# Performance work log

Measured on AMD Instinct MI355X. Metric: run time of the kernel, lower is better.

Reference implementation:

```python
import jax, jax.numpy as jnp
import numpy as np

N_PATHS = 8
T2_EFF = 0.5 * 100.0 + 0.5 * (100 // 50)  # p_dimer*T2_dimer + p_trimer*T2_trimer = 51.0
J_FREQ = 20.0


def setup_inputs() -> dict:
    key = jax.random.key(0)
    ks = jax.random.split(key, 5)
    B, D, H, P = 2048, 1024, 1024, N_PATHS
    return {
        "x": jax.random.normal(ks[0], (B, D), dtype=jnp.float32),
        "W_input": jax.random.normal(ks[1], (D, H), dtype=jnp.float32) * 0.1,
        "W_paths": jax.random.normal(ks[2], (P, H, H), dtype=jnp.float32) * 0.1,
        "J_coupling": jax.random.normal(ks[3], (P, P), dtype=jnp.float32) * 0.01,
        "coherent_state": jax.random.normal(ks[4], (B, P, H), dtype=jnp.float32),
        "t": jnp.ones((1,), dtype=jnp.float32),  # time_since_formation buffer
    }


def reference(x, W_input, W_paths, J_coupling, coherent_state, t):
    # base activation: [B, H]
    base = x @ W_input
    # all per-path matmuls batched into one einsum: [B, P, H]
    path_act = jnp.einsum("bh,phk->bpk", base, W_paths)
    # coherence decay gate (scalar, broadcasts)
    alpha = jnp.clip(jnp.exp(-t[0] / T2_EFF), 0.0, 1.0)
    superposition = alpha * coherent_state + (1.0 - alpha) * path_act
    # interference matrix from symmetrized J-coupling
    J_sym = 0.5 * (J_coupling + J_coupling.T)
    phase = 2.0 * jnp.pi * J_FREQ * t[0] / 1000.0
    interference = jax.nn.softmax(jnp.cos(phase * J_sym), axis=1)  # [P, P]
    # double-loop mixing == small matmul over path dim
    interfered = jnp.einsum("ij,bjh->bih", interference, superposition) / N_PATHS
    interfered = interfered * alpha  # coherence_factor == alpha
    # no measurement (default path): mean over paths
    return jnp.mean(interfered, axis=1)  # [B, H]
```

## Files before the change

### kernel.cpp

```cpp
#include <hip/hip_runtime.h>
#include <cstdint>


typedef __attribute__((ext_vector_type(8))) __bf16 bf16x8;
typedef __attribute__((ext_vector_type(4))) float f32x4;

__device__ __forceinline__ unsigned short f32_to_bf16_rne(float f) {
  unsigned int u = __float_as_uint(f);
  u += 0x7fffu + ((u >> 16) & 1u);
  return (unsigned short)(u >> 16);
}

__device__ __forceinline__ void load16_lds(const void* g, void* l) {
  __builtin_amdgcn_global_load_lds(
      (const __attribute__((address_space(1))) void*)g,
      (__attribute__((address_space(3))) void*)(unsigned int)(unsigned long long)l,
      16, 0, 0);
}

__device__ __forceinline__ void wave_scalars(const float* __restrict__ J,
                                             const float* __restrict__ t,
                                             float* w_out, float* alpha_out) {
  const int lane = threadIdx.x & 63;
  float tv = t[0];
  float alpha = fminf(fmaxf(expf(-tv / 51.0f), 0.0f), 1.0f);
  float phase = 2.0f * 3.14159265358979323846f * 20.0f * tv / 1000.0f;
  int i = lane >> 3, j = lane & 7;
  float jsym = 0.5f * (J[i * 8 + j] + J[j * 8 + i]);
  float e = expf(cosf(phase * jsym));
  float rs = e;
  rs += __shfl_xor(rs, 1);
  rs += __shfl_xor(rs, 2);
  rs += __shfl_xor(rs, 4);
  float p = e / rs;
  float cs = p;
  cs += __shfl_xor(cs, 8);
  cs += __shfl_xor(cs, 16);
  cs += __shfl_xor(cs, 32);
  *w_out = alpha * (1.0f / 64.0f) * cs;
  *alpha_out = alpha;
}

__global__ __launch_bounds__(256, 4) void k_prep(
    const float* __restrict__ x, const float* __restrict__ win,
    const float* __restrict__ wp, const float* __restrict__ J,
    const float* __restrict__ t, const float* __restrict__ coh,
    unsigned short* __restrict__ xb, unsigned short* __restrict__ winb,
    unsigned short* __restrict__ wefft, float* __restrict__ out) {
  const int blk = blockIdx.x;
  const int tid = threadIdx.x;
  const int lane = tid & 63;

  if (blk < 3072) {
    int idx = blk * 256 + tid;
    const float4* src;
    unsigned short* dst;
    int off;
    if (idx < 524288) { src = (const float4*)x;   dst = xb;   off = idx; }
    else              { src = (const float4*)win; dst = winb; off = idx - 524288; }
    float4 v = src[off];
    ushort4 o;
    o.x = f32_to_bf16_rne(v.x);
    o.y = f32_to_bf16_rne(v.y);
    o.z = f32_to_bf16_rne(v.z);
    o.w = f32_to_bf16_rne(v.w);
    ((ushort4*)dst)[off] = o;
  } else if (blk < 5120) {
    float wv, alpha;
    wave_scalars(J, t, &wv, &alpha);
    float wHI[8];
#pragma unroll
    for (int p = 0; p < 8; p++) wHI[p] = __shfl(wv, (lane & 56) | p) * alpha;
    int idx = (blk - 3072) * 256 + tid;
    int b = idx >> 8, hq = idx & 255;
    const f32x4* cb = (const f32x4*)(coh + (size_t)b * 8192) + hq;
    f32x4 acc = {0.f, 0.f, 0.f, 0.f};
#pragma unroll
    for (int p = 0; p < 8; p++) acc += wHI[p] * cb[p * 256];
    ((f32x4*)out)[idx] = acc;
  } else {
    __shared__ float lt[64][69];
    float wv, alpha;
    wave_scalars(J, t, &wv, &alpha);
    float wLO[8];
#pragma unroll
    for (int p = 0; p < 8; p++)
      wLO[p] = __shfl(wv, (lane & 56) | p) * (1.0f - alpha);
    const int q = blk - 5120;
    const int a0 = (q & 15) * 64;
    const int b0 = (q >> 4) * 64;
    const int rb = tid >> 4, c = tid & 15;
    f32x4 acc[4];
#pragma unroll
    for (int s = 0; s < 4; s++) acc[s] = {0.f, 0.f, 0.f, 0.f};
#pragma unroll
    for (int j = 0; j < 8; j++) {
      const float* base = wp + (size_t)j * 1024 * 1024 + b0 + c * 4;
      float wj = wLO[j];
#pragma unroll
      for (int s = 0; s < 4; s++) {
        f32x4 v = *(const f32x4*)(base + (size_t)(a0 + rb + 16 * s) * 1024);
        acc[s] += wj * v;
      }
    }
#pragma unroll
    for (int s = 0; s < 4; s++)
#pragma unroll
      for (int e = 0; e < 4; e++) lt[rb + 16 * s][c * 4 + e] = acc[s][e];
    __syncthreads();
    const int h2l = tid >> 2, h1g = (tid & 3) * 16;
    unsigned short* dst = wefft + (size_t)(b0 + h2l) * 1024 + a0 + h1g;
#pragma unroll
    for (int v4 = 0; v4 < 4; v4++) {
      ushort4 o;
      o.x = f32_to_bf16_rne(lt[h1g + v4 * 4 + 0][h2l]);
      o.y = f32_to_bf16_rne(lt[h1g + v4 * 4 + 1][h2l]);
      o.z = f32_to_bf16_rne(lt[h1g + v4 * 4 + 2][h2l]);
      o.w = f32_to_bf16_rne(lt[h1g + v4 * 4 + 3][h2l]);
      ((ushort4*)dst)[v4] = o;
    }
  }
}

template <int MAIN>
__global__ __launch_bounds__(256, 4) void k_gemm(
    const unsigned short* __restrict__ A, const unsigned short* __restrict__ B,
    float* __restrict__ outf, unsigned short* __restrict__ outb) {
  constexpr int K = 1024;
  constexpr int BK = 64;
  __shared__ alignas(16) unsigned short As[64 * BK];
  __shared__ alignas(16) unsigned short Bs[32 * BK];

  const int m0 = blockIdx.x * 64;
  const int n0 = blockIdx.y * 32;
  const int tid = threadIdx.x;
  const int wave = tid >> 6;
  const int lane = tid & 63;
  const int quad = lane >> 4;
  const int t16 = lane & 15;

  const int crow = lane >> 3;
  const int grp = lane & 7;
  const unsigned short* gA[2];
  unsigned short* lA[2];
#pragma unroll
  for (int c = 0; c < 2; c++) {
    int r = wave * 16 + c * 8 + crow;
    gA[c] = A + (size_t)(m0 + r) * K + (size_t)((grp ^ (r & 7)) * 8);
    lA[c] = As + (wave * 16 + c * 8) * BK + lane * 8;
  }
  const int rB = wave * 8 + crow;
  const unsigned short* gB = B + (size_t)(n0 + rB) * K + (size_t)((grp ^ (rB & 7)) * 8);
  unsigned short* lB = Bs + (wave * 8) * BK + lane * 8;

  const int ra = wave * 16 + t16;
  const unsigned short* pa[2];
  const unsigned short* pb[2][2];
#pragma unroll
  for (int kk = 0; kk < 2; kk++)
    pa[kk] = As + ra * BK + ((kk * 4 + quad) ^ (ra & 7)) * 8;
#pragma unroll
  for (int ni = 0; ni < 2; ni++) {
    int rb = ni * 16 + t16;
#pragma unroll
    for (int kk = 0; kk < 2; kk++)
      pb[ni][kk] = Bs + rb * BK + ((kk * 4 + quad) ^ (rb & 7)) * 8;
  }

  f32x4 acc[2] = {{0.f, 0.f, 0.f, 0.f}, {0.f, 0.f, 0.f, 0.f}};

  for (int kt = 0; kt < K; kt += BK) {
    __syncthreads();
    load16_lds(gA[0] + kt, lA[0]);
    load16_lds(gA[1] + kt, lA[1]);
    load16_lds(gB + kt, lB);
    __syncthreads();
#pragma unroll
    for (int kk = 0; kk < 2; kk++) {
      bf16x8 a = *(const bf16x8*)pa[kk];
      bf16x8 b0v = *(const bf16x8*)pb[0][kk];
      bf16x8 b1v = *(const bf16x8*)pb[1][kk];
      acc[0] = __builtin_amdgcn_mfma_f32_16x16x32_bf16(a, b0v, acc[0], 0, 0, 0);
      acc[1] = __builtin_amdgcn_mfma_f32_16x16x32_bf16(a, b1v, acc[1], 0, 0, 0);
    }
  }

#pragma unroll
  for (int r = 0; r < 4; r++) {
    const int m = m0 + wave * 16 + quad * 4 + r;
#pragma unroll
    for (int ni = 0; ni < 2; ni++) {
      const int n = n0 + ni * 16 + t16;
      const size_t idx = (size_t)m * 1024 + n;
      if constexpr (MAIN) {
        outf[idx] = outf[idx] + acc[ni][r];
      } else {
        outb[idx] = f32_to_bf16_rne(acc[ni][r]);
      }
    }
  }
}

extern "C" void kernel_launch(void* const* d_in, const int* in_sizes, int n_in,
                              void* d_out, int out_size, void* d_ws, size_t ws_size,
                              hipStream_t stream) {
  const float* x   = (const float*)d_in[0];
  const float* win = (const float*)d_in[1];
  const float* wp  = (const float*)d_in[2];
  const float* J   = (const float*)d_in[3];
  const float* coh = (const float*)d_in[4];
  const float* t   = (const float*)d_in[5];
  float* out = (float*)d_out;

  char* ws = (char*)d_ws;
  unsigned short* xb    = (unsigned short*)ws;
  unsigned short* winb  = (unsigned short*)(ws + 4u * 1024 * 1024);
  unsigned short* wefft = (unsigned short*)(ws + 6u * 1024 * 1024);
  unsigned short* wct   = (unsigned short*)(ws + 8u * 1024 * 1024);

  k_prep<<<5376, 256, 0, stream>>>(x, win, wp, J, t, coh, xb, winb, wefft, out);
  k_gemm<0><<<dim3(16, 32), 256, 0, stream>>>(wefft, winb, nullptr, wct);
  k_gemm<1><<<dim3(32, 32), 256, 0, stream>>>(xb, wct, out, nullptr);
}
```

Before: 162.3 us.

## Pre-swizzle bf16 operands into MFMA fragment layout and drop LDS staging in GEMMs

The prep kernel now writes x, W_input, the collapsed path weight and the intermediate product directly in a per-lane MFMA fragment order. This lets the GEMM kernels load bf16x8 operands straight from global memory with no LDS tiles or barriers. The GEMM tiles grow (64x64 and 128x64 per block, with several fragments per wave) and the prep grid is reduced by giving each block more work. The cost is extra LDS transposes in prep and reliance on cache for operand reuse across waves.

```diff
diff --git a/kernel.cpp b/kernel.cpp
--- a/kernel.cpp
+++ b/kernel.cpp
@@ -4,18 +4,12 @@
 
 typedef __attribute__((ext_vector_type(8))) __bf16 bf16x8;
 typedef __attribute__((ext_vector_type(4))) float f32x4;
-
-__device__ __forceinline__ unsigned short f32_to_bf16_rne(float f) {
+typedef unsigned short u16;
+
+__device__ __forceinline__ u16 f32_to_bf16_rne(float f) {
   unsigned int u = __float_as_uint(f);
   u += 0x7fffu + ((u >> 16) & 1u);
-  return (unsigned short)(u >> 16);
-}
-
-__device__ __forceinline__ void load16_lds(const void* g, void* l) {
-  __builtin_amdgcn_global_load_lds(
-      (const __attribute__((address_space(1))) void*)g,
-      (__attribute__((address_space(3))) void*)(unsigned int)(unsigned long long)l,
-      16, 0, 0);
+  return (u16)(u >> 16);
 }
 
 __device__ __forceinline__ void wave_scalars(const float* __restrict__ J,
@@ -41,162 +35,180 @@
   *alpha_out = alpha;
 }
 
-__global__ __launch_bounds__(256, 4) void k_prep(
+__global__ __launch_bounds__(256) void k_prep(
     const float* __restrict__ x, const float* __restrict__ win,
     const float* __restrict__ wp, const float* __restrict__ J,
     const float* __restrict__ t, const float* __restrict__ coh,
-    unsigned short* __restrict__ xb, unsigned short* __restrict__ winb,
-    unsigned short* __restrict__ wefft, float* __restrict__ out) {
+    u16* __restrict__ xfrag, u16* __restrict__ winfrag,
+    u16* __restrict__ wefrag, float* __restrict__ out) {
+  __shared__ __align__(16) char smem[33024];
   const int blk = blockIdx.x;
   const int tid = threadIdx.x;
   const int lane = tid & 63;
 
-  if (blk < 3072) {
-    int idx = blk * 256 + tid;
-    const float4* src;
-    unsigned short* dst;
-    int off;
-    if (idx < 524288) { src = (const float4*)x;   dst = xb;   off = idx; }
-    else              { src = (const float4*)win; dst = winb; off = idx - 524288; }
-    float4 v = src[off];
-    ushort4 o;
-    o.x = f32_to_bf16_rne(v.x);
-    o.y = f32_to_bf16_rne(v.y);
-    o.z = f32_to_bf16_rne(v.z);
-    o.w = f32_to_bf16_rne(v.w);
-    ((ushort4*)dst)[off] = o;
-  } else if (blk < 5120) {
+  if (blk < 256) {
+    float* lt = (float*)smem;
+    float wv, alpha;
+    wave_scalars(J, t, &wv, &alpha);
+    float wLO[8];
+#pragma unroll
+    for (int p = 0; p < 8; p++)
+      wLO[p] = __shfl(wv, (lane & 56) | p) * (1.0f - alpha);
+    const int a0 = (blk & 15) * 64;
+    const int b0 = (blk >> 4) * 64;
+    const int rb = tid >> 4, c = tid & 15;
+    f32x4 acc[4];
+#pragma unroll
+    for (int s = 0; s < 4; s++) acc[s] = (f32x4){0.f, 0.f, 0.f, 0.f};
+#pragma unroll
+    for (int j = 0; j < 8; j++) {
+      const float* base = wp + (size_t)j * 1048576 + b0 + c * 4;
+      float wj = wLO[j];
+#pragma unroll
+      for (int s = 0; s < 4; s++)
+        acc[s] += wj * *(const f32x4*)(base + (size_t)(a0 + rb + 16 * s) * 1024);
+    }
+#pragma unroll
+    for (int s = 0; s < 4; s++)
+#pragma unroll
+      for (int e = 0; e < 4; e++) lt[(rb + 16 * s) * 69 + c * 4 + e] = acc[s][e];
+    __syncthreads();
+#pragma unroll
+    for (int s2 = 0; s2 < 2; s2++) {
+      int idx = s2 * 256 + tid;
+      int lf = idx & 63, ktl = (idx >> 6) & 1, rtl = idx >> 7;
+      int h2l = rtl * 16 + (lf & 15);
+      int h1b = ktl * 32 + ((lf >> 4) << 3);
+      __align__(16) u16 o[8];
+#pragma unroll
+      for (int i = 0; i < 8; i++)
+        o[i] = f32_to_bf16_rne(lt[(h1b + i) * 69 + h2l]);
+      int rt = (b0 >> 4) + rtl, kt = (a0 >> 5) + ktl;
+      *(uint4*)(wefrag + ((size_t)(rt * 32 + kt) * 64 + lf) * 8) = *(const uint4*)o;
+    }
+  } else if (blk < 768) {
     float wv, alpha;
     wave_scalars(J, t, &wv, &alpha);
     float wHI[8];
 #pragma unroll
     for (int p = 0; p < 8; p++) wHI[p] = __shfl(wv, (lane & 56) | p) * alpha;
-    int idx = (blk - 3072) * 256 + tid;
-    int b = idx >> 8, hq = idx & 255;
-    const f32x4* cb = (const f32x4*)(coh + (size_t)b * 8192) + hq;
-    f32x4 acc = {0.f, 0.f, 0.f, 0.f};
-#pragma unroll
-    for (int p = 0; p < 8; p++) acc += wHI[p] * cb[p * 256];
-    ((f32x4*)out)[idx] = acc;
+    const f32x4* c4 = (const f32x4*)coh;
+    f32x4* o4 = (f32x4*)out;
+    const int base = (blk - 256) * 256 + tid;
+#pragma unroll
+    for (int u = 0; u < 4; u++) {
+      int idx = base + u * 131072;
+      int b = idx >> 8, hq = idx & 255;
+      const f32x4* cb = c4 + (size_t)b * 2048 + hq;
+      f32x4 acc = {0.f, 0.f, 0.f, 0.f};
+#pragma unroll
+      for (int p = 0; p < 8; p++) acc += wHI[p] * cb[p * 256];
+      o4[idx] = acc;
+    }
   } else {
-    __shared__ float lt[64][69];
-    float wv, alpha;
-    wave_scalars(J, t, &wv, &alpha);
-    float wLO[8];
-#pragma unroll
-    for (int p = 0; p < 8; p++)
-      wLO[p] = __shfl(wv, (lane & 56) | p) * (1.0f - alpha);
-    const int q = blk - 5120;
-    const int a0 = (q & 15) * 64;
-    const int b0 = (q >> 4) * 64;
-    const int rb = tid >> 4, c = tid & 15;
-    f32x4 acc[4];
-#pragma unroll
-    for (int s = 0; s < 4; s++) acc[s] = {0.f, 0.f, 0.f, 0.f};
-#pragma unroll
-    for (int j = 0; j < 8; j++) {
-      const float* base = wp + (size_t)j * 1024 * 1024 + b0 + c * 4;
-      float wj = wLO[j];
-#pragma unroll
-      for (int s = 0; s < 4; s++) {
-        f32x4 v = *(const f32x4*)(base + (size_t)(a0 + rb + 16 * s) * 1024);
-        acc[s] += wj * v;
+    const int cid = blk - 768;
+    const float* src;
+    u16* dst;
+    if (cid < 128) {
+      src = x + (size_t)cid * 16384;
+      dst = xfrag + (size_t)cid * 16384;
+    } else {
+      src = win + (size_t)(cid - 128) * 16384;
+      dst = winfrag + (size_t)(cid - 128) * 16384;
+    }
+    u16* ld = (u16*)smem;
+#pragma unroll
+    for (int i = 0; i < 16; i++) {
+      int idx = i * 256 + tid;
+      int row = idx >> 8, c4i = idx & 255;
+      f32x4 v = *(const f32x4*)(src + row * 1024 + c4i * 4);
+      ushort4 o;
+      o.x = f32_to_bf16_rne(v.x);
+      o.y = f32_to_bf16_rne(v.y);
+      o.z = f32_to_bf16_rne(v.z);
+      o.w = f32_to_bf16_rne(v.w);
+      *(ushort4*)(ld + row * 1032 + c4i * 4) = o;
+    }
+    __syncthreads();
+#pragma unroll
+    for (int s = 0; s < 8; s++) {
+      int idx = s * 256 + tid;
+      int lf = idx & 63, kt = idx >> 6;
+      int row = lf & 15, colb = kt * 32 + ((lf >> 4) << 3);
+      *(uint4*)(dst + (kt * 64 + lf) * 8) = *(const uint4*)(ld + row * 1032 + colb);
+    }
+  }
+}
+
+template <int FM, int RMW>
+__global__ __launch_bounds__(256) void k_fgemm(
+    const u16* __restrict__ Af, const u16* __restrict__ Bf,
+    float* __restrict__ outf, u16* __restrict__ ofrag) {
+  const int tid = threadIdx.x;
+  const int wave = tid >> 6, lane = tid & 63;
+  const int quad = lane >> 4, t16 = lane & 15;
+  const int m0 = blockIdx.x * (FM * 32);
+  const int n0 = blockIdx.y * 64;
+  const int wm = (wave >> 1) * (FM * 16);
+  const int wn = (wave & 1) * 32;
+  const u16* ap = Af + (size_t)(((m0 + wm) >> 4) * 32) * 512 + lane * 8;
+  const u16* bp = Bf + (size_t)(((n0 + wn) >> 4) * 32) * 512 + lane * 8;
+
+  f32x4 acc[FM][2];
+#pragma unroll
+  for (int mi = 0; mi < FM; mi++)
+#pragma unroll
+    for (int ni = 0; ni < 2; ni++) acc[mi][ni] = (f32x4){0.f, 0.f, 0.f, 0.f};
+
+#pragma unroll 4
+  for (int kt = 0; kt < 32; kt++) {
+    bf16x8 a[FM], b[2];
+#pragma unroll
+    for (int mi = 0; mi < FM; mi++)
+      a[mi] = *(const bf16x8*)(ap + (mi * 32 + kt) * 512);
+#pragma unroll
+    for (int ni = 0; ni < 2; ni++)
+      b[ni] = *(const bf16x8*)(bp + (ni * 32 + kt) * 512);
+#pragma unroll
+    for (int mi = 0; mi < FM; mi++)
+#pragma unroll
+      for (int ni = 0; ni < 2; ni++)
+        acc[mi][ni] = __builtin_amdgcn_mfma_f32_16x16x32_bf16(a[mi], b[ni],
+                                                              acc[mi][ni], 0, 0, 0);
+  }
+
+  if constexpr (RMW) {
+#pragma unroll
+    for (int mi = 0; mi < FM; mi++)
+#pragma unroll
+      for (int r = 0; r < 4; r++) {
+        size_t mrow = (size_t)(m0 + wm + mi * 16 + quad * 4 + r) * 1024;
+#pragma unroll
+        for (int ni = 0; ni < 2; ni++) {
+          size_t off = mrow + n0 + wn + ni * 16 + t16;
+          outf[off] += acc[mi][ni][r];
+        }
       }
-    }
-#pragma unroll
-    for (int s = 0; s < 4; s++)
-#pragma unroll
-      for (int e = 0; e < 4; e++) lt[rb + 16 * s][c * 4 + e] = acc[s][e];
+  } else {
+    __shared__ u16 ct[64 * 72];
+#pragma unroll
+    for (int mi = 0; mi < FM; mi++)
+#pragma unroll
+      for (int r = 0; r < 4; r++)
+#pragma unroll
+        for (int ni = 0; ni < 2; ni++)
+          ct[(wm + mi * 16 + quad * 4 + r) * 72 + wn + ni * 16 + t16] =
+              f32_to_bf16_rne(acc[mi][ni][r]);
     __syncthreads();
-    const int h2l = tid >> 2, h1g = (tid & 3) * 16;
-    unsigned short* dst = wefft + (size_t)(b0 + h2l) * 1024 + a0 + h1g;
-#pragma unroll
-    for (int v4 = 0; v4 < 4; v4++) {
-      ushort4 o;
-      o.x = f32_to_bf16_rne(lt[h1g + v4 * 4 + 0][h2l]);
-      o.y = f32_to_bf16_rne(lt[h1g + v4 * 4 + 1][h2l]);
-      o.z = f32_to_bf16_rne(lt[h1g + v4 * 4 + 2][h2l]);
-      o.w = f32_to_bf16_rne(lt[h1g + v4 * 4 + 3][h2l]);
-      ((ushort4*)dst)[v4] = o;
-    }
-  }
-}
-
-template <int MAIN>
-__global__ __launch_bounds__(256, 4) void k_gemm(
-    const unsigned short* __restrict__ A, const unsigned short* __restrict__ B,
-    float* __restrict__ outf, unsigned short* __restrict__ outb) {
-  constexpr int K = 1024;
-  constexpr int BK = 64;
-  __shared__ alignas(16) unsigned short As[64 * BK];
-  __shared__ alignas(16) unsigned short Bs[32 * BK];
-
-  const int m0 = blockIdx.x * 64;
-  const int n0 = blockIdx.y * 32;
-  const int tid = threadIdx.x;
-  const int wave = tid >> 6;
-  const int lane = tid & 63;
-  const int quad = lane >> 4;
-  const int t16 = lane & 15;
-
-  const int crow = lane >> 3;
-  const int grp = lane & 7;
-  const unsigned short* gA[2];
-  unsigned short* lA[2];
-#pragma unroll
-  for (int c = 0; c < 2; c++) {
-    int r = wave * 16 + c * 8 + crow;
-    gA[c] = A + (size_t)(m0 + r) * K + (size_t)((grp ^ (r & 7)) * 8);
-    lA[c] = As + (wave * 16 + c * 8) * BK + lane * 8;
-  }
-  const int rB = wave * 8 + crow;
-  const unsigned short* gB = B + (size_t)(n0 + rB) * K + (size_t)((grp ^ (rB & 7)) * 8);
-  unsigned short* lB = Bs + (wave * 8) * BK + lane * 8;
-
-  const int ra = wave * 16 + t16;
-  const unsigned short* pa[2];
-  const unsigned short* pb[2][2];
-#pragma unroll
-  for (int kk = 0; kk < 2; kk++)
-    pa[kk] = As + ra * BK + ((kk * 4 + quad) ^ (ra & 7)) * 8;
-#pragma unroll
-  for (int ni = 0; ni < 2; ni++) {
-    int rb = ni * 16 + t16;
-#pragma unroll
-    for (int kk = 0; kk < 2; kk++)
-      pb[ni][kk] = Bs + rb * BK + ((kk * 4 + quad) ^ (rb & 7)) * 8;
-  }
-
-  f32x4 acc[2] = {{0.f, 0.f, 0.f, 0.f}, {0.f, 0.f, 0.f, 0.f}};
-
-  for (int kt = 0; kt < K; kt += BK) {
-    __syncthreads();
-    load16_lds(gA[0] + kt, lA[0]);
-    load16_lds(gA[1] + kt, lA[1]);
-    load16_lds(gB + kt, lB);
-    __syncthreads();
-#pragma unroll
-    for (int kk = 0; kk < 2; kk++) {
-      bf16x8 a = *(const bf16x8*)pa[kk];
-      bf16x8 b0v = *(const bf16x8*)pb[0][kk];
-      bf16x8 b1v = *(const bf16x8*)pb[1][kk];
-      acc[0] = __builtin_amdgcn_mfma_f32_16x16x32_bf16(a, b0v, acc[0], 0, 0, 0);
-      acc[1] = __builtin_amdgcn_mfma_f32_16x16x32_bf16(a, b1v, acc[1], 0, 0, 0);
-    }
-  }
-
-#pragma unroll
-  for (int r = 0; r < 4; r++) {
-    const int m = m0 + wave * 16 + quad * 4 + r;
-#pragma unroll
-    for (int ni = 0; ni < 2; ni++) {
-      const int n = n0 + ni * 16 + t16;
-      const size_t idx = (size_t)m * 1024 + n;
-      if constexpr (MAIN) {
-        outf[idx] = outf[idx] + acc[ni][r];
-      } else {
-        outb[idx] = f32_to_bf16_rne(acc[ni][r]);
-      }
+#pragma unroll
+    for (int s2 = 0; s2 < 2; s2++) {
+      int idx = s2 * 256 + tid;
+      int lf = idx & 63, ktl = (idx >> 6) & 1, rtl = idx >> 7;
+      int rowl = rtl * 16 + (lf & 15);
+      int colb = ktl * 32 + ((lf >> 4) << 3);
+      int rt = (m0 >> 4) + rtl, kt = (n0 >> 5) + ktl;
+      *(uint4*)(ofrag + ((size_t)(rt * 32 + kt) * 64 + lf) * 8) =
+          *(const uint4*)(ct + rowl * 72 + colb);
     }
   }
 }
@@ -213,12 +225,14 @@
   float* out = (float*)d_out;
 
   char* ws = (char*)d_ws;
-  unsigned short* xb    = (unsigned short*)ws;
-  unsigned short* winb  = (unsigned short*)(ws + 4u * 1024 * 1024);
-  unsigned short* wefft = (unsigned short*)(ws + 6u * 1024 * 1024);
-  unsigned short* wct   = (unsigned short*)(ws + 8u * 1024 * 1024);
-
-  k_prep<<<5376, 256, 0, stream>>>(x, win, wp, J, t, coh, xb, winb, wefft, out);
-  k_gemm<0><<<dim3(16, 32), 256, 0, stream>>>(wefft, winb, nullptr, wct);
-  k_gemm<1><<<dim3(32, 32), 256, 0, stream>>>(xb, wct, out, nullptr);
-}
+  u16* xfrag   = (u16*)ws;
+  u16* winfrag = (u16*)(ws + 4u * 1024 * 1024);
+  u16* wefrag  = (u16*)(ws + 6u * 1024 * 1024);
+  u16* wctfrag = (u16*)(ws + 8u * 1024 * 1024);
+
+  k_prep<<<960, 256, 0, stream>>>(x, win, wp, J, t, coh, xfrag, winfrag, wefrag,
+                                  out);
+  k_fgemm<2, 0><<<dim3(16, 16), 256, 0, stream>>>(wefrag, winfrag, nullptr,
+                                                  wctfrag);
+  k_fgemm<4, 1><<<dim3(16, 16), 256, 0, stream>>>(xfrag, wctfrag, out, nullptr);
+}
```

Result: slower. 170.1 us (+4.8%).
